# Performance work log

Measured on AMD Instinct MI355X. Metric: run time of the kernel, lower is better.

The kernel has to match this reference:

```python
import jax, jax.numpy as jnp
import numpy as np

FEATURE_DIM = 768
LAMBDA_REG = 0.01
NUM_ITERS = 5
LR = 0.1
SIGMA = 2.0
MARGIN = 1.0
BN_EPS = 1e-5


def setup_inputs() -> dict:
    key = jax.random.key(0)
    ks = jax.random.split(key, 10)
    B, D = 32, FEATURE_DIM
    search_features = jax.random.normal(ks[0], (B, D, 32, 32), dtype=jnp.float32)
    target_features = jax.random.normal(ks[1], (B, D, 16, 16), dtype=jnp.float32)
    target_mask = jax.random.uniform(ks[2], (B, 1, 16, 16), dtype=jnp.float32)
    conv_w = jax.random.normal(ks[3], (D, D), dtype=jnp.float32) * (1.0 / np.sqrt(D))
    conv_b = jax.random.normal(ks[4], (D,), dtype=jnp.float32) * 0.01
    bn_gamma = jnp.ones((D,), dtype=jnp.float32)
    bn_beta = jnp.zeros((D,), dtype=jnp.float32)
    bn_mean = jax.random.normal(ks[5], (D,), dtype=jnp.float32) * 0.01
    bn_var = jax.random.uniform(ks[6], (D,), dtype=jnp.float32, minval=0.5, maxval=1.5)
    filter_init = jax.random.normal(ks[7], (1, D, 1, 1), dtype=jnp.float32) * 0.01
    return {
        "search_features": search_features,
        "target_features": target_features,
        "target_mask": target_mask,
        "conv_w": conv_w,
        "conv_b": conv_b,
        "bn_gamma": bn_gamma,
        "bn_beta": bn_beta,
        "bn_mean": bn_mean,
        "bn_var": bn_var,
        "filter_init": filter_init,
    }


def _proj(x, conv_w, conv_b, bn_gamma, bn_beta, bn_mean, bn_var):
    # 1x1 conv == channel-wise GEMM, then BatchNorm (eval mode, running stats)
    y = jnp.einsum('bdhw,ed->behw', x, conv_w) + conv_b[None, :, None, None]
    inv_std = bn_gamma / jnp.sqrt(bn_var + BN_EPS)
    return (y - bn_mean[None, :, None, None]) * inv_std[None, :, None, None] + bn_beta[None, :, None, None]


def _gaussian_label(mask):
    B, _, H, W = mask.shape
    yy, xx = jnp.meshgrid(jnp.arange(H, dtype=jnp.float32), jnp.arange(W, dtype=jnp.float32), indexing='ij')
    yy = yy[None, None]  # (1,1,H,W)
    xx = xx[None, None]
    msum = jnp.clip(mask.sum(axis=(2, 3), keepdims=True), 1.0)
    cy = (mask * yy).sum(axis=(2, 3), keepdims=True) / msum
    cx = (mask * xx).sum(axis=(2, 3), keepdims=True) / msum
    return jnp.exp(-((xx - cx) ** 2 + (yy - cy) ** 2) / (2.0 * SIGMA ** 2))


def reference(search_features, target_features, target_mask, conv_w, conv_b,
              bn_gamma, bn_beta, bn_mean, bn_var, filter_init):
    sp = _proj(search_features, conv_w, conv_b, bn_gamma, bn_beta, bn_mean, bn_var)
    tp = _proj(target_features, conv_w, conv_b, bn_gamma, bn_beta, bn_mean, bn_var)
    B = tp.shape[0]
    label = _gaussian_label(target_mask)  # (B,1,H',W')
    f = jnp.broadcast_to(filter_init, (B,) + filter_init.shape[1:])  # (B,D,1,1)
    for _ in range(NUM_ITERS):
        response = (tp * f).sum(axis=1, keepdims=True)  # (B,1,H',W')
        loss = jnp.maximum(MARGIN - response * label, 0.0)
        grad = jnp.where(loss > 0, -label * target_mask, 0.0)
        grad = grad.mean(axis=(2, 3), keepdims=True)  # (B,1,1,1), broadcasts over D
        f = f - LR * (grad + LAMBDA_REG * f)
    return (sp * f).sum(axis=1, keepdims=True)  # (B,1,H,W)
```

## Files before the change

### kernel.cpp

```cpp
#include <hip/hip_runtime.h>
#include <math.h>

#define DD   768
#define BB   32
#define NTP  256
#define NSP  1024
#define NT   (BB*NTP)
#define NS   (BB*NSP)
#define ECH  16
#define CHE  (DD/ECH)
#define NQ   4
#define QCH  (DD/NQ)

#define OFF_UP  0
#define OFF_VP  (OFF_UP + ECH*DD)
#define OFF_K   (OFF_VP + ECH*DD)
#define OFF_TR0 (OFF_K + 64)
#define OFF_TS0 (OFF_TR0 + NQ*NT)
#define OFF_SR  (OFF_TS0 + NQ*NT)
#define OFF_SS  (OFF_SR + NQ*NS)

#define A5 0.99500999000499900f

__global__ void k_prep(const float* __restrict__ w, const float* __restrict__ cb,
                       const float* __restrict__ gamma, const float* __restrict__ beta,
                       const float* __restrict__ mean, const float* __restrict__ var,
                       const float* __restrict__ fi, float* __restrict__ ws) {
    int bx = blockIdx.x;
    int t = threadIdx.x;
    if (bx < ECH) {
        __shared__ float wu[CHE], wv[CHE];
        if (t < CHE) {
            int e = bx * CHE + t;
            float inv = gamma[e] / sqrtf(var[e] + 1e-5f);
            wv[t] = inv;
            wu[t] = inv * fi[e];
        }
        __syncthreads();
        if (t < 192) {
            const float4* w4 = (const float4*)w;
            float4 Ru = {0,0,0,0}, Rv = {0,0,0,0};
            #pragma unroll
            for (int j = 0; j < CHE; ++j) {
                float4 x = w4[(size_t)(bx * CHE + j) * 192 + t];
                float a = wu[j], b = wv[j];
                Ru.x += x.x * a; Ru.y += x.y * a; Ru.z += x.z * a; Ru.w += x.w * a;
                Rv.x += x.x * b; Rv.y += x.y * b; Rv.z += x.z * b; Rv.w += x.w * b;
            }
            *(float4*)(ws + OFF_UP + bx * DD + t * 4) = Ru;
            *(float4*)(ws + OFF_VP + bx * DD + t * 4) = Rv;
        }
    } else {
        __shared__ float r1[256], r2[256];
        float a1 = 0.f, a2 = 0.f;
        for (int e = t; e < DD; e += 256) {
            float inv = gamma[e] / sqrtf(var[e] + 1e-5f);
            float x = (cb[e] - mean[e]) * inv + beta[e];
            a1 += x * fi[e];
            a2 += x;
        }
        r1[t] = a1; r2[t] = a2;
        __syncthreads();
        for (int s = 128; s > 0; s >>= 1) {
            if (t < s) { r1[t] += r1[t + s]; r2[t] += r2[t + s]; }
            __syncthreads();
        }
        if (t == 0) { ws[OFF_K] = r1[0]; ws[OFF_K + 1] = r2[0]; }
    }
}

__global__ __launch_bounds__(256, 5) void k_big(const float* __restrict__ sf,
                                                const float* __restrict__ tf,
                                                float* __restrict__ ws) {
    int bx = blockIdx.x;
    int t = threadIdx.x;
    int pxf4 = t & 31, sub = t >> 5;

    int b, q, cq; bool isS;
    if (bx < 1024) { isS = true;  cq = bx & 3; q = (bx >> 2) & 7; b = bx >> 5; }
    else           { isS = false; int u = bx - 1024; cq = u & 3; q = (u >> 2) & 1; b = u >> 3; }

    __shared__ float su[QCH], sv[QCH];
    if (t < QCH / 4) {
        float4 U = {0,0,0,0}, V = {0,0,0,0};
        #pragma unroll
        for (int ec = 0; ec < ECH; ++ec) {
            float4 a = ((const float4*)(ws + OFF_UP))[ec * 192 + cq * 48 + t];
            float4 c = ((const float4*)(ws + OFF_VP))[ec * 192 + cq * 48 + t];
            U.x += a.x; U.y += a.y; U.z += a.z; U.w += a.w;
            V.x += c.x; V.y += c.y; V.z += c.z; V.w += c.w;
        }
        ((float4*)su)[t] = U;
        ((float4*)sv)[t] = V;
    }
    __syncthreads();

    const float4* base;
    int STR;
    float4 *oR, *oS;
    if (isS) {
        base = (const float4*)sf + ((size_t)b * DD + cq * QCH + sub * 24) * (NSP/4) + q * 32 + pxf4;
        STR = NSP / 4;
        int g4 = b * 256 + q * 32 + pxf4;
        oR = (float4*)(ws + OFF_SR) + cq * (NS/4) + g4;
        oS = (float4*)(ws + OFF_SS) + cq * (NS/4) + g4;
    } else {
        base = (const float4*)tf + ((size_t)b * DD + cq * QCH + sub * 24) * (NTP/4) + q * 32 + pxf4;
        STR = NTP / 4;
        int g4 = b * 64 + q * 32 + pxf4;
        oR = (float4*)(ws + OFF_TR0) + cq * (NT/4) + g4;
        oS = (float4*)(ws + OFF_TS0) + cq * (NT/4) + g4;
    }

    float4 accR = {0,0,0,0}, accS = {0,0,0,0};
    float4 buf[8];
    #pragma unroll
    for (int k = 0; k < 8; ++k) buf[k] = base[(size_t)k * STR];
    #pragma unroll
    for (int g = 1; g < 3; ++g) {
        float4 nxt[8];
        #pragma unroll
        for (int k = 0; k < 8; ++k) nxt[k] = base[(size_t)(g * 8 + k) * STR];
        #pragma unroll
        for (int k = 0; k < 8; ++k) {
            int ch = sub * 24 + (g - 1) * 8 + k;
            float u = su[ch], v = sv[ch];
            accR.x += buf[k].x * u; accR.y += buf[k].y * u; accR.z += buf[k].z * u; accR.w += buf[k].w * u;
            accS.x += buf[k].x * v; accS.y += buf[k].y * v; accS.z += buf[k].z * v; accS.w += buf[k].w * v;
            buf[k] = nxt[k];
        }
    }
    #pragma unroll
    for (int k = 0; k < 8; ++k) {
        int ch = sub * 24 + 16 + k;
        float u = su[ch], v = sv[ch];
        accR.x += buf[k].x * u; accR.y += buf[k].y * u; accR.z += buf[k].z * u; accR.w += buf[k].w * u;
        accS.x += buf[k].x * v; accS.y += buf[k].y * v; accS.z += buf[k].z * v; accS.w += buf[k].w * v;
    }

    __shared__ float4 redR[8][32], redS[8][32];
    redR[sub][pxf4] = accR; redS[sub][pxf4] = accS;
    __syncthreads();
    for (int s = 4; s > 0; s >>= 1) {
        if (sub < s) {
            float4 a = redR[sub + s][pxf4], m = redR[sub][pxf4];
            m.x += a.x; m.y += a.y; m.z += a.z; m.w += a.w; redR[sub][pxf4] = m;
            float4 c = redS[sub + s][pxf4], n = redS[sub][pxf4];
            n.x += c.x; n.y += c.y; n.z += c.z; n.w += c.w; redS[sub][pxf4] = n;
        }
        __syncthreads();
    }
    if (sub == 0) { *oR = redR[0][pxf4]; *oS = redS[0][pxf4]; }
}

__global__ void k_final(const float* __restrict__ mask, const float* __restrict__ ws,
                        float* __restrict__ out) {
    int b = blockIdx.x;
    int p = threadIdx.x;
    int lane = p & 63, wv = p >> 6;
    int h = p >> 4, w = p & 15;
    float K1 = ws[OFF_K], K2 = ws[OFF_K + 1];
    float r0 = K1, s0 = K2;
    #pragma unroll
    for (int cq = 0; cq < NQ; ++cq) {
        r0 += ws[OFF_TR0 + cq * NT + b * 256 + p];
        s0 += ws[OFF_TS0 + cq * NT + b * 256 + p];
    }
    float m = mask[b * 256 + p];
    __shared__ float cross[4];
    auto bsum = [&](float v) -> float {
        #pragma unroll
        for (int o = 32; o > 0; o >>= 1) v += __shfl_xor(v, o, 64);
        if (lane == 0) cross[wv] = v;
        __syncthreads();
        float r = cross[0] + cross[1] + cross[2] + cross[3];
        __syncthreads();
        return r;
    };
    float msum = bsum(m);
    float sy = bsum(m * (float)h);
    float sx = bsum(m * (float)w);
    msum = fmaxf(msum, 1.0f);
    float cy = sy / msum, cx = sx / msum;
    float dx = (float)w - cx, dy = (float)h - cy;
    float label = expf(-(dx * dx + dy * dy) * 0.125f);
    float A = 1.0f, c = 0.0f;
    const float decay = 1.0f - 0.1f * 0.01f;
    #pragma unroll
    for (int it = 0; it < 5; ++it) {
        float resp = A * r0 + c * s0;
        float gc = (1.0f - resp * label > 0.0f) ? (-label * m) : 0.0f;
        float g = bsum(gc) * (1.0f / 256.0f);
        c = decay * c - 0.1f * g;
        A *= decay;
    }
    int g4 = b * 256 + p;
    float4 R = {K1, K1, K1, K1}, S = {K2, K2, K2, K2};
    #pragma unroll
    for (int cq = 0; cq < NQ; ++cq) {
        float4 a = ((const float4*)(ws + OFF_SR))[cq * (NS/4) + g4];
        float4 d = ((const float4*)(ws + OFF_SS))[cq * (NS/4) + g4];
        R.x += a.x; R.y += a.y; R.z += a.z; R.w += a.w;
        S.x += d.x; S.y += d.y; S.z += d.z; S.w += d.w;
    }
    float4 o;
    o.x = A5 * R.x + c * S.x;
    o.y = A5 * R.y + c * S.y;
    o.z = A5 * R.z + c * S.z;
    o.w = A5 * R.w + c * S.w;
    ((float4*)out)[g4] = o;
}

extern "C" void kernel_launch(void* const* d_in, const int* in_sizes, int n_in,
                              void* d_out, int out_size, void* d_ws, size_t ws_size,
                              hipStream_t stream) {
    const float* sf    = (const float*)d_in[0];
    const float* tf    = (const float*)d_in[1];
    const float* mask  = (const float*)d_in[2];
    const float* w     = (const float*)d_in[3];
    const float* cb    = (const float*)d_in[4];
    const float* gamma = (const float*)d_in[5];
    const float* beta  = (const float*)d_in[6];
    const float* mean  = (const float*)d_in[7];
    const float* var   = (const float*)d_in[8];
    const float* fi    = (const float*)d_in[9];
    float* out = (float*)d_out;
    float* ws  = (float*)d_ws;

    k_prep <<<ECH + 1, 256, 0, stream>>>(w, cb, gamma, beta, mean, var, fi, ws);
    k_big  <<<1280,    256, 0, stream>>>(sf, tf, ws);
    k_final<<<BB,      256, 0, stream>>>(mask, ws, out);
}
```

Measured before the change: 34.61 us.

## Split channels into eighths with 64-wide pixel tiles and deeper prefetch in k_big

Changes the k_big work decomposition: each block now covers 1/8 of the channels (96) across 64 float4 pixel columns with 4 sub-groups of 24 channels, instead of 1/4 of the channels across 32 pixel columns with 8 sub-groups. The load pipeline keeps 12 float4s in flight per thread in a rolling buffer. The in-block reduction drops from three rounds to two, and the U/V preamble is split across two thread groups. In exchange, the partial-result workspace doubles, and k_final must read and sum 8 partials instead of 4, adding extra global traffic.

```diff
diff --git a/kernel.cpp b/kernel.cpp
--- a/kernel.cpp
+++ b/kernel.cpp
@@ -9,16 +9,16 @@
 #define NS   (BB*NSP)
 #define ECH  16
 #define CHE  (DD/ECH)
-#define NQ   4
-#define QCH  (DD/NQ)
+#define NO   8
+#define OCH  (DD/NO)
 
 #define OFF_UP  0
 #define OFF_VP  (OFF_UP + ECH*DD)
 #define OFF_K   (OFF_VP + ECH*DD)
 #define OFF_TR0 (OFF_K + 64)
-#define OFF_TS0 (OFF_TR0 + NQ*NT)
-#define OFF_SR  (OFF_TS0 + NQ*NT)
-#define OFF_SS  (OFF_SR + NQ*NS)
+#define OFF_TS0 (OFF_TR0 + NO*NT)
+#define OFF_SR  (OFF_TS0 + NO*NT)
+#define OFF_SS  (OFF_SR + NO*NS)
 
 #define A5 0.99500999000499900f
 
@@ -74,24 +74,30 @@
                                                 float* __restrict__ ws) {
     int bx = blockIdx.x;
     int t = threadIdx.x;
-    int pxf4 = t & 31, sub = t >> 5;
-
-    int b, q, cq; bool isS;
-    if (bx < 1024) { isS = true;  cq = bx & 3; q = (bx >> 2) & 7; b = bx >> 5; }
-    else           { isS = false; int u = bx - 1024; cq = u & 3; q = (u >> 2) & 1; b = u >> 3; }
-
-    __shared__ float su[QCH], sv[QCH];
-    if (t < QCH / 4) {
-        float4 U = {0,0,0,0}, V = {0,0,0,0};
+    int pxf4 = t & 63, sub = t >> 6;
+
+    int b, q, oct; bool isS;
+    if (bx < 1024) { isS = true;  oct = bx & 7; q = (bx >> 3) & 3; b = bx >> 5; }
+    else           { isS = false; int u = bx - 1024; oct = u & 7; q = 0; b = u >> 3; }
+
+    __shared__ float su[OCH], sv[OCH];
+    if (t < 24) {
+        float4 U = {0,0,0,0};
         #pragma unroll
         for (int ec = 0; ec < ECH; ++ec) {
-            float4 a = ((const float4*)(ws + OFF_UP))[ec * 192 + cq * 48 + t];
-            float4 c = ((const float4*)(ws + OFF_VP))[ec * 192 + cq * 48 + t];
+            float4 a = ((const float4*)(ws + OFF_UP))[ec * 192 + oct * 24 + t];
             U.x += a.x; U.y += a.y; U.z += a.z; U.w += a.w;
+        }
+        ((float4*)su)[t] = U;
+    } else if (t < 48) {
+        int j = t - 24;
+        float4 V = {0,0,0,0};
+        #pragma unroll
+        for (int ec = 0; ec < ECH; ++ec) {
+            float4 c = ((const float4*)(ws + OFF_VP))[ec * 192 + oct * 24 + j];
             V.x += c.x; V.y += c.y; V.z += c.z; V.w += c.w;
         }
-        ((float4*)su)[t] = U;
-        ((float4*)sv)[t] = V;
+        ((float4*)sv)[j] = V;
     }
     __syncthreads();
 
@@ -99,58 +105,49 @@
     int STR;
     float4 *oR, *oS;
     if (isS) {
-        base = (const float4*)sf + ((size_t)b * DD + cq * QCH + sub * 24) * (NSP/4) + q * 32 + pxf4;
+        base = (const float4*)sf + ((size_t)b * DD + oct * OCH + sub * 24) * (NSP/4) + q * 64 + pxf4;
         STR = NSP / 4;
-        int g4 = b * 256 + q * 32 + pxf4;
-        oR = (float4*)(ws + OFF_SR) + cq * (NS/4) + g4;
-        oS = (float4*)(ws + OFF_SS) + cq * (NS/4) + g4;
+        int g4 = b * 256 + q * 64 + pxf4;
+        oR = (float4*)(ws + OFF_SR) + oct * (NS/4) + g4;
+        oS = (float4*)(ws + OFF_SS) + oct * (NS/4) + g4;
     } else {
-        base = (const float4*)tf + ((size_t)b * DD + cq * QCH + sub * 24) * (NTP/4) + q * 32 + pxf4;
+        base = (const float4*)tf + ((size_t)b * DD + oct * OCH + sub * 24) * (NTP/4) + pxf4;
         STR = NTP / 4;
-        int g4 = b * 64 + q * 32 + pxf4;
-        oR = (float4*)(ws + OFF_TR0) + cq * (NT/4) + g4;
-        oS = (float4*)(ws + OFF_TS0) + cq * (NT/4) + g4;
+        int g4 = b * 64 + pxf4;
+        oR = (float4*)(ws + OFF_TR0) + oct * (NT/4) + g4;
+        oS = (float4*)(ws + OFF_TS0) + oct * (NT/4) + g4;
     }
 
     float4 accR = {0,0,0,0}, accS = {0,0,0,0};
-    float4 buf[8];
-    #pragma unroll
-    for (int k = 0; k < 8; ++k) buf[k] = base[(size_t)k * STR];
-    #pragma unroll
-    for (int g = 1; g < 3; ++g) {
-        float4 nxt[8];
-        #pragma unroll
-        for (int k = 0; k < 8; ++k) nxt[k] = base[(size_t)(g * 8 + k) * STR];
-        #pragma unroll
-        for (int k = 0; k < 8; ++k) {
-            int ch = sub * 24 + (g - 1) * 8 + k;
-            float u = su[ch], v = sv[ch];
-            accR.x += buf[k].x * u; accR.y += buf[k].y * u; accR.z += buf[k].z * u; accR.w += buf[k].w * u;
-            accS.x += buf[k].x * v; accS.y += buf[k].y * v; accS.z += buf[k].z * v; accS.w += buf[k].w * v;
-            buf[k] = nxt[k];
-        }
-    }
-    #pragma unroll
-    for (int k = 0; k < 8; ++k) {
-        int ch = sub * 24 + 16 + k;
-        float u = su[ch], v = sv[ch];
-        accR.x += buf[k].x * u; accR.y += buf[k].y * u; accR.z += buf[k].z * u; accR.w += buf[k].w * u;
-        accS.x += buf[k].x * v; accS.y += buf[k].y * v; accS.z += buf[k].z * v; accS.w += buf[k].w * v;
-    }
-
-    __shared__ float4 redR[8][32], redS[8][32];
+    float4 buf[12];
+    #pragma unroll
+    for (int k = 0; k < 12; ++k) buf[k] = base[(size_t)k * STR];
+    #pragma unroll
+    for (int i = 0; i < 24; ++i) {
+        float4 v = buf[i % 12];
+        if (i < 12) buf[i % 12] = base[(size_t)(i + 12) * STR];
+        float u = su[sub * 24 + i], vb = sv[sub * 24 + i];
+        accR.x += v.x * u;  accR.y += v.y * u;  accR.z += v.z * u;  accR.w += v.w * u;
+        accS.x += v.x * vb; accS.y += v.y * vb; accS.z += v.z * vb; accS.w += v.w * vb;
+    }
+
+    __shared__ float4 redR[4][64], redS[4][64];
     redR[sub][pxf4] = accR; redS[sub][pxf4] = accS;
     __syncthreads();
-    for (int s = 4; s > 0; s >>= 1) {
-        if (sub < s) {
-            float4 a = redR[sub + s][pxf4], m = redR[sub][pxf4];
-            m.x += a.x; m.y += a.y; m.z += a.z; m.w += a.w; redR[sub][pxf4] = m;
-            float4 c = redS[sub + s][pxf4], n = redS[sub][pxf4];
-            n.x += c.x; n.y += c.y; n.z += c.z; n.w += c.w; redS[sub][pxf4] = n;
-        }
-        __syncthreads();
-    }
-    if (sub == 0) { *oR = redR[0][pxf4]; *oS = redS[0][pxf4]; }
+    if (sub < 2) {
+        float4 a = redR[sub + 2][pxf4], m = redR[sub][pxf4];
+        m.x += a.x; m.y += a.y; m.z += a.z; m.w += a.w; redR[sub][pxf4] = m;
+        float4 c = redS[sub + 2][pxf4], n = redS[sub][pxf4];
+        n.x += c.x; n.y += c.y; n.z += c.z; n.w += c.w; redS[sub][pxf4] = n;
+    }
+    __syncthreads();
+    if (sub == 0) {
+        float4 a = redR[1][pxf4], m = redR[0][pxf4];
+        m.x += a.x; m.y += a.y; m.z += a.z; m.w += a.w;
+        float4 c = redS[1][pxf4], n = redS[0][pxf4];
+        n.x += c.x; n.y += c.y; n.z += c.z; n.w += c.w;
+        *oR = m; *oS = n;
+    }
 }
 
 __global__ void k_final(const float* __restrict__ mask, const float* __restrict__ ws,
@@ -162,9 +159,9 @@
     float K1 = ws[OFF_K], K2 = ws[OFF_K + 1];
     float r0 = K1, s0 = K2;
     #pragma unroll
-    for (int cq = 0; cq < NQ; ++cq) {
-        r0 += ws[OFF_TR0 + cq * NT + b * 256 + p];
-        s0 += ws[OFF_TS0 + cq * NT + b * 256 + p];
+    for (int o = 0; o < NO; ++o) {
+        r0 += ws[OFF_TR0 + o * NT + b * 256 + p];
+        s0 += ws[OFF_TS0 + o * NT + b * 256 + p];
     }
     float m = mask[b * 256 + p];
     __shared__ float cross[4];
@@ -197,9 +194,9 @@
     int g4 = b * 256 + p;
     float4 R = {K1, K1, K1, K1}, S = {K2, K2, K2, K2};
     #pragma unroll
-    for (int cq = 0; cq < NQ; ++cq) {
-        float4 a = ((const float4*)(ws + OFF_SR))[cq * (NS/4) + g4];
-        float4 d = ((const float4*)(ws + OFF_SS))[cq * (NS/4) + g4];
+    for (int o = 0; o < NO; ++o) {
+        float4 a = ((const float4*)(ws + OFF_SR))[o * (NS/4) + g4];
+        float4 d = ((const float4*)(ws + OFF_SS))[o * (NS/4) + g4];
         R.x += a.x; R.y += a.y; R.z += a.z; R.w += a.w;
         S.x += d.x; S.y += d.y; S.z += d.z; S.w += d.w;
     }
```

New measurement: 35.14 us. Within noise of the previous version (+1.5%).
